# Performance work log

Hardware: AMD Instinct MI355X
Metric: run time of the kernel (lower is better)

The kernel has to match this reference:

```python
import jax, jax.numpy as jnp
import numpy as np

H, W, HEADS, DIM_HEAD, SLICE = 256, 256, 8, 64, 64
SCALE = DIM_HEAD ** -0.5


def _conv(x_nhwc, w_hwio, b):
    y = jax.lax.conv_general_dilated(
        x_nhwc, w_hwio, window_strides=(1, 1), padding='SAME',
        dimension_numbers=('NHWC', 'HWIO', 'NHWC'))
    return y + b


def setup_inputs() -> dict:
    key = jax.random.key(0)
    ks = jax.random.split(key, 13)
    B, N, C, inner = 2, H * W, 128, HEADS * DIM_HEAD
    s = lambda k, shp, sc: jax.random.normal(k, shp, jnp.float32) * sc
    return {
        'x': s(ks[0], (B, N, C), 1.0),
        'Wfx': s(ks[1], (3, 3, C, inner), 0.05),
        'bfx': s(ks[2], (inner,), 0.02),
        'Wx': s(ks[3], (3, 3, C, inner), 0.05),
        'bx': s(ks[4], (inner,), 0.02),
        'Wslice': s(ks[5], (SLICE, DIM_HEAD), 0.1),
        'bslice': s(ks[6], (SLICE,), 0.02),
        'temperature': jnp.ones((1, HEADS, 1, 1), jnp.float32) * 0.5,
        'Wq': s(ks[7], (DIM_HEAD, DIM_HEAD), 0.1),
        'Wk': s(ks[8], (DIM_HEAD, DIM_HEAD), 0.1),
        'Wv': s(ks[9], (DIM_HEAD, DIM_HEAD), 0.1),
        'Wout': s(ks[10], (C, inner), 0.05),
        'bout': s(ks[11], (C,), 0.02),
    }


def reference(x, Wfx, bfx, Wx, bx, Wslice, bslice, temperature, Wq, Wk, Wv, Wout, bout):
    B, N, C = x.shape
    xg = x.reshape(B, H, W, C)                       # NHWC grid
    # conv QKV-style projections -> [B, heads, N, dim_head]
    def to_heads(y):
        return y.reshape(B, N, HEADS, DIM_HEAD).transpose(0, 2, 1, 3)
    fx_mid = to_heads(_conv(xg, Wfx, bfx))           # [B,h,N,d]
    x_mid = to_heads(_conv(xg, Wx, bx))              # [B,h,N,d]
    # slice assignment weights: softmax over slices with clamped temperature
    temp = jnp.clip(temperature, 0.1, 5.0)           # [1,h,1,1]
    logits = (jnp.einsum('bhnd,gd->bhng', x_mid, Wslice) + bslice) / temp
    slice_weights = jax.nn.softmax(logits, axis=-1)  # [B,h,N,G]
    slice_norm = slice_weights.sum(axis=2)           # [B,h,G]
    slice_token = jnp.einsum('bhnc,bhng->bhgc', fx_mid, slice_weights)
    slice_token = slice_token / (slice_norm + 1e-5)[..., None]  # [B,h,G,d]
    # small attention over slice tokens
    q = jnp.einsum('bhgd,ed->bhge', slice_token, Wq)
    k = jnp.einsum('bhgd,ed->bhge', slice_token, Wk)
    v = jnp.einsum('bhgd,ed->bhge', slice_token, Wv)
    attn = jax.nn.softmax(jnp.einsum('bhge,bhfe->bhgf', q, k) * SCALE, axis=-1)
    out_slice = jnp.einsum('bhgf,bhfe->bhge', attn, v)           # [B,h,G,d]
    # scatter back to tokens
    out_x = jnp.einsum('bhgc,bhng->bhnc', out_slice, slice_weights)
    out_x = out_x.transpose(0, 2, 1, 3).reshape(B, N, HEADS * DIM_HEAD)
    return jnp.einsum('bni,oi->bno', out_x, Wout) + bout
```

## Files before the change

### kernel.cpp

```cpp
#include <hip/hip_runtime.h>


typedef _Float16 f16;
typedef _Float16 f16x8 __attribute__((ext_vector_type(8)));
typedef _Float16 f16x4 __attribute__((ext_vector_type(4)));
typedef float    f32x4 __attribute__((ext_vector_type(4)));

static const size_t OFF_PADX = 0;
static const size_t OFF_WCAT = 17040384;
static const size_t OFF_ST   = 19399680;
static const size_t OFF_NORM = 19530752;
static const size_t OFF_OS   = 19532800;
static const size_t OFF_PT   = 19663872;
static const size_t OFF_XMID = 19794944;
static const size_t OFF_FXT  = 86903808;

__device__ __forceinline__ void ldsdma16(f16* lds, const f16* g) {
  __builtin_amdgcn_global_load_lds((__attribute__((address_space(1))) void*)g,
                                   (__attribute__((address_space(3))) void*)lds,
                                   16, 0, 0);
}

__global__ __launch_bounds__(256) void pad_kernel(const float* __restrict__ xb,
                                                  f16* __restrict__ padx) {
  int idx = blockIdx.x * 256 + threadIdx.x;
  if (idx >= 258 * 258 * 16) return;
  int c8 = (idx & 15) * 8;
  int r  = idx >> 4;
  int jp = r % 258;
  int ip = r / 258;
  f16x8 v;
  if (ip == 0 || ip == 257 || jp == 0 || jp == 257) {
#pragma unroll
    for (int j = 0; j < 8; ++j) v[j] = (f16)0.0f;
  } else {
    const float* src = xb + ((size_t)(ip - 1) * 256 + (jp - 1)) * 128 + c8;
#pragma unroll
    for (int j = 0; j < 8; ++j) v[j] = (f16)src[j];
  }
  *(f16x8*)(padx + (size_t)r * 128 + c8) = v;
}

__global__ __launch_bounds__(256) void prepw_kernel(const float* __restrict__ Wfx,
                                                    const float* __restrict__ Wx,
                                                    f16* __restrict__ wcat) {
  int idx = blockIdx.x * 256 + threadIdx.x;
  if (idx >= 9 * 1024 * 128) return;
  int ci = idx & 127;
  int t  = idx >> 7;
  int co = t & 1023;
  int tap = t >> 10;
  float v = (co < 512) ? Wfx[(size_t)(tap * 128 + ci) * 512 + co]
                       : Wx[(size_t)(tap * 128 + ci) * 512 + (co - 512)];
  wcat[idx] = (f16)v;
}

__global__ __launch_bounds__(256, 2) void conv_kernel(const f16* __restrict__ padx,
                                                      const f16* __restrict__ wcat,
                                                      const float* __restrict__ bfx,
                                                      const float* __restrict__ bx,
                                                      f16* __restrict__ xmid,
                                                      f16* __restrict__ fxT) {
  __shared__ f16 smem[33024];
  f16* As0 = smem;
  f16* As1 = smem + 8320;
  f16* Bs0 = smem + 16640;
  f16* Bs1 = smem + 24832;
  int tid = threadIdx.x;
  int nt = blockIdx.x & 7;
  int mt = blockIdx.x >> 3;
  int i  = mt >> 1;
  int j0 = (mt & 1) * 128;
  int n0 = nt * 128;
  int lane = tid & 63, wave = tid >> 6;
  int ln15 = lane & 15, quad = lane >> 4;
  int wm = wave & 1, wn = wave >> 1;

  f32x4 acc[4][4] = {};

  auto stageA = [&](int di, int kc, f16* dst) {
#pragma unroll
    for (int ph = 0; ph < 5; ++ph) {
      int s = ph * 256 + tid;
      if (ph < 4 || s < 1040) {
        int rr = s >> 3;
        int qq = ((s & 7) ^ (rr & 7)) * 8;
        ldsdma16(&dst[(ph * 256 + wave * 64) * 8],
                 padx + ((size_t)(i + di) * 258 + j0 + rr) * 128 + kc + qq);
      }
    }
  };
  auto stageB = [&](int tap, int kc, f16* dst) {
#pragma unroll
    for (int ph = 0; ph < 4; ++ph) {
      int s = ph * 256 + tid;
      int rr = s >> 3;
      int qq = ((s & 7) ^ (rr & 7)) * 8;
      ldsdma16(&dst[(ph * 256 + wave * 64) * 8],
               wcat + ((size_t)(tap * 1024 + n0 + rr)) * 128 + kc + qq);
    }
  };
  auto computePhase = [&](int dj, const f16* A, const f16* B) {
#pragma unroll
    for (int ks = 0; ks < 2; ++ks) {
      int q = ks * 4 + quad;
      f16x8 af[4], bfr[4];
#pragma unroll
      for (int xx = 0; xx < 4; ++xx) {
        int t  = dj + wm * 64 + xx * 16 + ln15;
        int rb = wn * 64 + xx * 16 + ln15;
        af[xx]  = *(const f16x8*)(&A[t * 64 + ((q ^ (t & 7)) * 8)]);
        bfr[xx] = *(const f16x8*)(&B[rb * 64 + ((q ^ (rb & 7)) * 8)]);
      }
      __builtin_amdgcn_s_setprio(1);
#pragma unroll
      for (int mf = 0; mf < 4; ++mf)
#pragma unroll
        for (int nf = 0; nf < 4; ++nf)
          acc[mf][nf] = __builtin_amdgcn_mfma_f32_16x16x32_f16(af[mf], bfr[nf],
                                                               acc[mf][nf], 0, 0, 0);
      __builtin_amdgcn_s_setprio(0);
    }
  };

  stageA(0, 0, As0);
  stageB(0, 0, Bs0);
  __syncthreads();

#pragma unroll
  for (int p = 0; p < 18; ++p) {
    int dj   = p % 3;
    int dikc = p / 3;
    if (p + 1 < 18) {
      int np = p + 1;
      int ndj = np % 3, ndikc = np / 3;
      int ndi = ndikc >> 1, nkc = (ndikc & 1) * 64;
      stageB(ndi * 3 + ndj, nkc, (np & 1) ? Bs1 : Bs0);
      if (ndj == 0) stageA(ndi, nkc, (ndikc & 1) ? As1 : As0);
    }
    computePhase(dj, (dikc & 1) ? As1 : As0, (p & 1) ? Bs1 : Bs0);
    __syncthreads();
  }

  size_t token0 = (size_t)i * 256 + j0;
  if (nt < 4) {
    f16* tile = smem;
#pragma unroll
    for (int nf = 0; nf < 4; ++nf) {
      int colLoc = wn * 64 + nf * 16 + ln15;
      float bias = bfx[n0 + colLoc];
#pragma unroll
      for (int mf = 0; mf < 4; ++mf) {
        int tokBase = wm * 64 + mf * 16 + quad * 4;
        f16x4 pk;
#pragma unroll
        for (int v = 0; v < 4; ++v) pk[v] = (f16)(acc[mf][nf][v] + bias);
        *(f16x4*)(&tile[colLoc * 136 + tokBase]) = pk;
      }
    }
    __syncthreads();
#pragma unroll
    for (int it2 = 0; it2 < 8; ++it2) {
      int s = it2 * 256 + tid;
      int c = s >> 4, t8 = s & 15;
      f16x8 vv = *(const f16x8*)(&tile[c * 136 + t8 * 8]);
      *(f16x8*)(fxT + (size_t)(n0 + c) * 65536 + token0 + t8 * 8) = vv;
    }
  } else {
#pragma unroll
    for (int nf = 0; nf < 4; ++nf) {
      int col = n0 + wn * 64 + nf * 16 + ln15;
      float bias = bx[col - 512];
#pragma unroll
      for (int mf = 0; mf < 4; ++mf) {
        int rbase = wm * 64 + mf * 16 + quad * 4;
#pragma unroll
        for (int v = 0; v < 4; ++v)
          xmid[(size_t)(token0 + rbase + v) * 512 + (col - 512)] =
              (f16)(acc[mf][nf][v] + bias);
      }
    }
  }
}

#define WS_S 72
#define WT_S 264
__global__ __launch_bounds__(256, 2) void slice_kernel(f16* __restrict__ xmid,
                                                       const f16* __restrict__ fxT,
                                                       const float* __restrict__ Wslice,
                                                       const float* __restrict__ bslice,
                                                       const float* __restrict__ temperature,
                                                       float* __restrict__ ST,
                                                       float* __restrict__ snorm) {
  __shared__ f16 Ws[64 * WS_S];
  __shared__ f16 Wt[64 * WT_S];
  __shared__ float red[64 * 65];
  __shared__ float redn[64];
  int tid = threadIdx.x;
  int h = blockIdx.x >> 6;
  int chunk = blockIdx.x & 63;
  int tok0 = chunk * 1024;
  int lane = tid & 63, wave = tid >> 6;
  int ln15 = lane & 15, quad = lane >> 4;

  for (int s = tid; s < 4096; s += 256)
    Ws[(s >> 6) * WS_S + (s & 63)] = (f16)Wslice[s];
  if (tid < 64) redn[tid] = 0.f;
  float tc = temperature[h];
  tc = fminf(fmaxf(tc, 0.1f), 5.0f);
  float invt = 1.0f / tc;
  float bsv[4];
#pragma unroll
  for (int nf = 0; nf < 4; ++nf) bsv[nf] = bslice[nf * 16 + ln15];
  __syncthreads();

  f32x4 acc2[4][4] = {};
  float naccv[4] = {};

  for (int it = 0; it < 4; ++it) {
    int tsub = it * 256 + wave * 64;
    f32x4 accA[4][4] = {};
#pragma unroll
    for (int kq = 0; kq < 2; ++kq) {
      f16x8 bf[4];
#pragma unroll
      for (int nf = 0; nf < 4; ++nf)
        bf[nf] = *(const f16x8*)(&Ws[(nf * 16 + ln15) * WS_S + kq * 32 + quad * 8]);
#pragma unroll
      for (int mf = 0; mf < 4; ++mf) {
        f16x8 af = *(const f16x8*)(xmid + (size_t)(tok0 + tsub + mf * 16 + ln15) * 512 +
                                   h * 64 + kq * 32 + quad * 8);
#pragma unroll
        for (int nf = 0; nf < 4; ++nf)
          accA[mf][nf] = __builtin_amdgcn_mfma_f32_16x16x32_f16(af, bf[nf], accA[mf][nf],
                                                                0, 0, 0);
      }
    }
#pragma unroll
    for (int mf = 0; mf < 4; ++mf) {
#pragma unroll
      for (int v = 0; v < 4; ++v) {
        float l[4];
#pragma unroll
        for (int nf = 0; nf < 4; ++nf) l[nf] = (accA[mf][nf][v] + bsv[nf]) * invt;
        float lm = fmaxf(fmaxf(l[0], l[1]), fmaxf(l[2], l[3]));
#pragma unroll
        for (int off = 1; off < 16; off <<= 1) lm = fmaxf(lm, __shfl_xor(lm, off, 64));
        float e[4], ssum = 0.f;
#pragma unroll
        for (int nf = 0; nf < 4; ++nf) { e[nf] = __expf(l[nf] - lm); ssum += e[nf]; }
#pragma unroll
        for (int off = 1; off < 16; off <<= 1) ssum += __shfl_xor(ssum, off, 64);
        float winv = 1.0f / ssum;
        int t_loc = tsub + mf * 16 + quad * 4 + v;
        int t_str = wave * 64 + mf * 16 + quad * 4 + v;
        f16* wrow = xmid + (size_t)(tok0 + t_loc) * 512 + h * 64;
#pragma unroll
        for (int nf = 0; nf < 4; ++nf) {
          float w = e[nf] * winv;
          naccv[nf] += w;
          f16 wh = (f16)w;
          wrow[nf * 16 + ln15] = wh;
          Wt[(nf * 16 + ln15) * WT_S + t_str] = wh;
        }
      }
    }
#pragma unroll
    for (int kq = 0; kq < 2; ++kq) {
      int kof = wave * 64 + kq * 32 + quad * 8;
      f16x8 bfB[4];
#pragma unroll
      for (int nf = 0; nf < 4; ++nf)
        bfB[nf] = *(const f16x8*)(fxT + (size_t)(h * 64 + nf * 16 + ln15) * 65536 +
                                  tok0 + it * 256 + kof);
#pragma unroll
      for (int mf = 0; mf < 4; ++mf) {
        f16x8 afB = *(const f16x8*)(&Wt[(mf * 16 + ln15) * WT_S + kof]);
#pragma unroll
        for (int nf = 0; nf < 4; ++nf)
          acc2[mf][nf] = __builtin_amdgcn_mfma_f32_16x16x32_f16(afB, bfB[nf],
                                                                acc2[mf][nf], 0, 0, 0);
      }
    }
  }

#pragma unroll
  for (int nf = 0; nf < 4; ++nf) atomicAdd(&redn[nf * 16 + ln15], naccv[nf]);

  for (int s = 0; s < 4; ++s) {
    if (wave == s) {
#pragma unroll
      for (int mf = 0; mf < 4; ++mf)
#pragma unroll
        for (int nf = 0; nf < 4; ++nf)
#pragma unroll
          for (int v = 0; v < 4; ++v) {
            int g = mf * 16 + quad * 4 + v;
            int d = nf * 16 + ln15;
            if (s == 0) red[g * 65 + d] = acc2[mf][nf][v];
            else        red[g * 65 + d] += acc2[mf][nf][v];
          }
    }
    __syncthreads();
  }
  float* stp = ST + (size_t)h * 4096;
  for (int s2 = tid; s2 < 4096; s2 += 256)
    atomicAdd(&stp[s2], red[(s2 >> 6) * 65 + (s2 & 63)]);
  if (tid < 64) atomicAdd(&snorm[h * 64 + tid], redn[tid]);
}

__global__ __launch_bounds__(256) void attn_kernel(const float* __restrict__ ST,
                                                   const float* __restrict__ snorm,
                                                   const float* __restrict__ Wq,
                                                   const float* __restrict__ Wk,
                                                   const float* __restrict__ Wv,
                                                   float* __restrict__ OS) {
  int h = blockIdx.x;
  __shared__ float tok[64 * 65];
  __shared__ float qs[64 * 65];
  __shared__ float ksm[64 * 65];
  __shared__ f16 vsm[64 * 65];
  int tid = threadIdx.x;
  const float* stp = ST + (size_t)h * 4096;
  const float* snp = snorm + (size_t)h * 64;
  for (int s = tid; s < 4096; s += 256) {
    int g = s >> 6, d = s & 63;
    tok[g * 65 + d] = stp[s] / (snp[g] + 1e-5f);
  }
  __syncthreads();
  int g = tid >> 2, p16 = (tid & 3) * 16;
  for (int e0 = 0; e0 < 16; ++e0) {
    int e = p16 + e0;
    const float* wq = Wq + e * 64;
    const float* wk = Wk + e * 64;
    const float* wv = Wv + e * 64;
    float aq = 0, ak = 0, av = 0;
#pragma unroll 8
    for (int d = 0; d < 64; ++d) {
      float tv = tok[g * 65 + d];
      aq += tv * wq[d];
      ak += tv * wk[d];
      av += tv * wv[d];
    }
    qs[g * 65 + e] = aq;
    ksm[g * 65 + e] = ak;
    vsm[g * 65 + e] = (f16)av;
  }
  __syncthreads();
  float* sc = tok;
  for (int f0 = 0; f0 < 16; ++f0) {
    int f = p16 + f0;
    float s = 0;
#pragma unroll 8
    for (int e = 0; e < 64; ++e) s += qs[g * 65 + e] * ksm[f * 65 + e];
    sc[g * 65 + f] = s * 0.125f;
  }
  __syncthreads();
  if (tid < 64) {
    float m = -1e30f;
    for (int f = 0; f < 64; ++f) m = fmaxf(m, sc[tid * 65 + f]);
    float ssum = 0;
    for (int f = 0; f < 64; ++f) {
      float e = __expf(sc[tid * 65 + f] - m);
      sc[tid * 65 + f] = e;
      ssum += e;
    }
    float inv = 1.0f / ssum;
    for (int f = 0; f < 64; ++f) sc[tid * 65 + f] *= inv;
  }
  __syncthreads();
  for (int e0 = 0; e0 < 16; ++e0) {
    int e = p16 + e0;
    float o = 0;
#pragma unroll 8
    for (int f = 0; f < 64; ++f) o += sc[g * 65 + f] * (float)vsm[f * 65 + e];
    OS[(size_t)h * 4096 + g * 64 + e] = o;
  }
}

__global__ __launch_bounds__(256) void pt_kernel(const float* __restrict__ OS,
                                                 const float* __restrict__ Wout,
                                                 f16* __restrict__ PT) {
  int h = blockIdx.x;
  __shared__ float os[64 * 65];
  int tid = threadIdx.x;
  for (int s = tid; s < 4096; s += 256) os[(s >> 6) * 65 + (s & 63)] = OS[(size_t)h * 4096 + s];
  __syncthreads();
  int o = tid >> 1, gh = (tid & 1) * 32;
  const float* wr = Wout + (size_t)o * 512 + h * 64;
  float wreg[64];
#pragma unroll
  for (int d = 0; d < 64; ++d) wreg[d] = wr[d];
  for (int gg = 0; gg < 32; ++gg) {
    int g = gh + gg;
    float s = 0;
#pragma unroll
    for (int d = 0; d < 64; ++d) s += os[g * 65 + d] * wreg[d];
    PT[(size_t)o * 512 + h * 64 + g] = (f16)s;
  }
}

__global__ __launch_bounds__(256, 2) void final_kernel(const f16* __restrict__ xmid,
                                                       const f16* __restrict__ PT,
                                                       const float* __restrict__ bout,
                                                       float* __restrict__ outb) {
  __shared__ f16 As[128 * 64];
  __shared__ f16 Bs[128 * 64];
  int tid = threadIdx.x;
  int tok0 = blockIdx.x << 7;
  int lane = tid & 63, wave = tid >> 6;
  int ln15 = lane & 15, quad = lane >> 4;
  int wm = wave & 1, wn = wave >> 1;
  int rr[4], qq8[4];
#pragma unroll
  for (int ph = 0; ph < 4; ++ph) {
    int s = ph * 256 + tid;
    rr[ph] = s >> 3;
    qq8[ph] = ((s & 7) ^ (rr[ph] & 7)) * 8;
  }
  int wbase = wave * 512;
  f32x4 acc[4][4] = {};
  const f16* aB = xmid + (size_t)tok0 * 512;
  const f16* bB = PT;
  for (int kc = 0; kc < 512; kc += 64) {
#pragma unroll
    for (int ph = 0; ph < 4; ++ph) {
      ldsdma16(&As[ph * 2048 + wbase], aB + (size_t)rr[ph] * 512 + kc + qq8[ph]);
      ldsdma16(&Bs[ph * 2048 + wbase], bB + (size_t)rr[ph] * 512 + kc + qq8[ph]);
    }
    __syncthreads();
#pragma unroll
    for (int ks = 0; ks < 2; ++ks) {
      f16x8 af[4], bfr[4];
      int q = ks * 4 + quad;
#pragma unroll
      for (int xx = 0; xx < 4; ++xx) {
        int ra = wm * 64 + xx * 16 + ln15;
        int rb = wn * 64 + xx * 16 + ln15;
        af[xx]  = *(const f16x8*)(&As[ra * 64 + (q ^ (ra & 7)) * 8]);
        bfr[xx] = *(const f16x8*)(&Bs[rb * 64 + (q ^ (rb & 7)) * 8]);
      }
#pragma unroll
      for (int mf = 0; mf < 4; ++mf)
#pragma unroll
        for (int nf = 0; nf < 4; ++nf)
          acc[mf][nf] = __builtin_amdgcn_mfma_f32_16x16x32_f16(af[mf], bfr[nf],
                                                               acc[mf][nf], 0, 0, 0);
    }
    __syncthreads();
  }
#pragma unroll
  for (int nf = 0; nf < 4; ++nf) {
    int col = wn * 64 + nf * 16 + ln15;
    float bo = bout[col];
#pragma unroll
    for (int mf = 0; mf < 4; ++mf) {
      int rbase = wm * 64 + mf * 16 + quad * 4;
#pragma unroll
      for (int v = 0; v < 4; ++v)
        outb[(size_t)(tok0 + rbase + v) * 128 + col] = acc[mf][nf][v] + bo;
    }
  }
}

extern "C" void kernel_launch(void* const* d_in, const int* in_sizes, int n_in,
                              void* d_out, int out_size, void* d_ws, size_t ws_size,
                              hipStream_t stream) {
  const float* x    = (const float*)d_in[0];
  const float* Wfx  = (const float*)d_in[1];
  const float* bfx  = (const float*)d_in[2];
  const float* Wx   = (const float*)d_in[3];
  const float* bx   = (const float*)d_in[4];
  const float* Wsl  = (const float*)d_in[5];
  const float* bsl  = (const float*)d_in[6];
  const float* temp = (const float*)d_in[7];
  const float* Wq   = (const float*)d_in[8];
  const float* Wk   = (const float*)d_in[9];
  const float* Wv   = (const float*)d_in[10];
  const float* Wout = (const float*)d_in[11];
  const float* bout = (const float*)d_in[12];
  float* out = (float*)d_out;
  char* ws = (char*)d_ws;

  f16*  padx = (f16*)(ws + OFF_PADX);
  f16*  wcat = (f16*)(ws + OFF_WCAT);
  float* ST  = (float*)(ws + OFF_ST);
  float* nrm = (float*)(ws + OFF_NORM);
  float* OS  = (float*)(ws + OFF_OS);
  f16*  PT   = (f16*)(ws + OFF_PT);
  f16*  xmid = (f16*)(ws + OFF_XMID);
  f16*  fxT  = (f16*)(ws + OFF_FXT);

  prepw_kernel<<<4608, 256, 0, stream>>>(Wfx, Wx, wcat);
  for (int b = 0; b < 2; ++b) {
    const float* xb = x + (size_t)b * 65536 * 128;
    float* outb = out + (size_t)b * 65536 * 128;
    (void)hipMemsetAsync(ws + OFF_ST, 0, 131072 + 2048, stream);
    pad_kernel<<<4161, 256, 0, stream>>>(xb, padx);
    conv_kernel<<<4096, 256, 0, stream>>>(padx, wcat, bfx, bx, xmid, fxT);
    slice_kernel<<<512, 256, 0, stream>>>(xmid, fxT, Wsl, bsl, temp, ST, nrm);
    attn_kernel<<<8, 256, 0, stream>>>(ST, nrm, Wq, Wk, Wv, OS);
    pt_kernel<<<8, 256, 0, stream>>>(OS, Wout, PT);
    final_kernel<<<512, 256, 0, stream>>>(xmid, PT, bout, outb);
  }
}
```

Before: 830.0 us.

## Double-buffer final GEMM LDS tiles and remap conv block order

The final projection GEMM now double-buffers its A/B tiles in LDS, so the next k-chunk's async global-to-LDS loads overlap the current chunk's MFMAs. It also raises wave priority around the MFMA block. The conv kernel remaps blockIdx so consecutive blocks share the same n-tile rather than cycling through all 8 n-tiles, which changes how L2 is reused across in-flight blocks. Doubling LDS use in the final kernel may cut occupancy, and the remap may hurt reuse of the padded input.

Result: slower. 849.8 us (+2.4%).

```diff
diff --git a/kernel.cpp b/kernel.cpp
--- a/kernel.cpp
+++ b/kernel.cpp
@@ -67,8 +67,9 @@
   f16* Bs0 = smem + 16640;
   f16* Bs1 = smem + 24832;
   int tid = threadIdx.x;
-  int nt = blockIdx.x & 7;
-  int mt = blockIdx.x >> 3;
+  int wg = (blockIdx.x & 7) * 512 + (blockIdx.x >> 3);
+  int nt = wg & 7;
+  int mt = wg >> 3;
   int i  = mt >> 1;
   int j0 = (mt & 1) * 128;
   int n0 = nt * 128;
@@ -404,8 +405,11 @@
                                                        const f16* __restrict__ PT,
                                                        const float* __restrict__ bout,
                                                        float* __restrict__ outb) {
-  __shared__ f16 As[128 * 64];
-  __shared__ f16 Bs[128 * 64];
+  __shared__ f16 smem[32768];
+  f16* As0 = smem;
+  f16* As1 = smem + 8192;
+  f16* Bs0 = smem + 16384;
+  f16* Bs1 = smem + 24576;
   int tid = threadIdx.x;
   int tok0 = blockIdx.x << 7;
   int lane = tid & 63, wave = tid >> 6;
@@ -422,13 +426,23 @@
   f32x4 acc[4][4] = {};
   const f16* aB = xmid + (size_t)tok0 * 512;
   const f16* bB = PT;
-  for (int kc = 0; kc < 512; kc += 64) {
+
+  auto stage = [&](int kc, f16* dA, f16* dB) {
 #pragma unroll
     for (int ph = 0; ph < 4; ++ph) {
-      ldsdma16(&As[ph * 2048 + wbase], aB + (size_t)rr[ph] * 512 + kc + qq8[ph]);
-      ldsdma16(&Bs[ph * 2048 + wbase], bB + (size_t)rr[ph] * 512 + kc + qq8[ph]);
-    }
-    __syncthreads();
+      ldsdma16(&dA[ph * 2048 + wbase], aB + (size_t)rr[ph] * 512 + kc + qq8[ph]);
+      ldsdma16(&dB[ph * 2048 + wbase], bB + (size_t)rr[ph] * 512 + kc + qq8[ph]);
+    }
+  };
+
+  stage(0, As0, Bs0);
+  __syncthreads();
+#pragma unroll
+  for (int kci = 0; kci < 8; ++kci) {
+    if (kci + 1 < 8)
+      stage((kci + 1) * 64, (kci & 1) ? As0 : As1, (kci & 1) ? Bs0 : Bs1);
+    const f16* A = (kci & 1) ? As1 : As0;
+    const f16* B = (kci & 1) ? Bs1 : Bs0;
 #pragma unroll
     for (int ks = 0; ks < 2; ++ks) {
       f16x8 af[4], bfr[4];
@@ -437,15 +451,17 @@
       for (int xx = 0; xx < 4; ++xx) {
         int ra = wm * 64 + xx * 16 + ln15;
         int rb = wn * 64 + xx * 16 + ln15;
-        af[xx]  = *(const f16x8*)(&As[ra * 64 + (q ^ (ra & 7)) * 8]);
-        bfr[xx] = *(const f16x8*)(&Bs[rb * 64 + (q ^ (rb & 7)) * 8]);
-      }
+        af[xx]  = *(const f16x8*)(&A[ra * 64 + (q ^ (ra & 7)) * 8]);
+        bfr[xx] = *(const f16x8*)(&B[rb * 64 + (q ^ (rb & 7)) * 8]);
+      }
+      __builtin_amdgcn_s_setprio(1);
 #pragma unroll
       for (int mf = 0; mf < 4; ++mf)
 #pragma unroll
         for (int nf = 0; nf < 4; ++nf)
           acc[mf][nf] = __builtin_amdgcn_mfma_f32_16x16x32_f16(af[mf], bfr[nf],
                                                                acc[mf][nf], 0, 0, 0);
+      __builtin_amdgcn_s_setprio(0);
     }
     __syncthreads();
   }
```
